# Kernel optimization log

Hardware: AMD Instinct MI355X
Metric: run time of the kernel (lower is better)

Reference implementation:

```python
import jax, jax.numpy as jnp
import numpy as np

B, N, D, E, K = 4, 4096, 768, 8, 2
H = 4 * D
LN_EPS = 1e-5


def setup_inputs() -> dict:
    key = jax.random.key(0)
    ks = jax.random.split(key, 9)
    s_d = 1.0 / np.sqrt(D)
    s_h = 1.0 / np.sqrt(H)
    return {
        "x": jax.random.normal(ks[0], (B, N, D), dtype=jnp.float32),
        "router_w": jax.random.normal(ks[1], (D, E), dtype=jnp.float32) * s_d,
        "router_b": jnp.zeros((E,), dtype=jnp.float32),
        "w1": jax.random.normal(ks[2], (E, D, H), dtype=jnp.float32) * s_d,
        "b1": jnp.zeros((E, H), dtype=jnp.float32),
        "w2": jax.random.normal(ks[3], (E, H, D), dtype=jnp.float32) * s_h,
        "b2": jnp.zeros((E, D), dtype=jnp.float32),
        "gamma": jnp.ones((D,), dtype=jnp.float32),
        "beta": jnp.zeros((D,), dtype=jnp.float32),
    }


def reference(x, router_w, router_b, w1, b1, w2, b2, gamma, beta):
    # Router logits and top-k gating (softmax over top-k values, in fp32)
    logits = jnp.einsum("bnd,de->bne", x, router_w) + router_b
    topv, topi = jax.lax.top_k(logits, K)                       # [B,N,K]
    w = jax.nn.softmax(topv.astype(jnp.float32), axis=-1).astype(x.dtype)
    # Per-token per-expert combine weight: [B,N,E]
    onehot = (topi[..., None] == jnp.arange(E)).astype(x.dtype)  # [B,N,K,E]
    we = jnp.einsum("bnk,bnke->bne", w, onehot)
    # Dense per-expert FFN, weighted combine (loop over small fixed E)
    out = jnp.zeros_like(x)
    for e in range(E):
        h = jax.nn.gelu(jnp.einsum("bnd,dh->bnh", x, w1[e]) + b1[e],
                        approximate=False)                      # exact GELU like torch
        y_e = jnp.einsum("bnh,hd->bnd", h, w2[e]) + b2[e]
        out = out + y_e * we[..., e:e + 1]
    # Residual + LayerNorm
    y = x + out
    mu = jnp.mean(y, axis=-1, keepdims=True)
    var = jnp.mean((y - mu) ** 2, axis=-1, keepdims=True)
    return (y - mu) * jax.lax.rsqrt(var + LN_EPS) * gamma + beta
```

## Files before the change

### kernel.cpp

```cpp
#include <hip/hip_runtime.h>
#include <hip/hip_bf16.h>
#include <math.h>

#define T_TOK 16384
#define DIM 768
#define NE 8
#define HID 3072
#define PADT 33792
#define CHUNK 8192
#define NCHUNK 5
#define NSLOT (T_TOK * 2)

typedef unsigned short u16;
typedef __attribute__((ext_vector_type(8))) short bf16x8;
typedef __attribute__((ext_vector_type(4))) float f32x4;

__device__ __forceinline__ u16 f2bf(float f) {
  union { float f; unsigned u; } v; v.f = f;
  unsigned r = v.u + 0x7FFF + ((v.u >> 16) & 1);
  return (u16)(r >> 16);
}

__device__ __forceinline__ float bf2f(u16 u) {
  union { unsigned u; float f; } v; v.u = ((unsigned)u) << 16; return v.f;
}

__device__ __forceinline__ void async16(void* lds, const void* g) {
  __builtin_amdgcn_global_load_lds((const __attribute__((address_space(1))) void*)g,
                                   (__attribute__((address_space(3))) void*)lds, 16, 0, 0);
}

__device__ __forceinline__ float gelu_f(float v) {
  float z = fabsf(v) * 0.70710678118f;
  float t = __builtin_amdgcn_rcpf(1.f + 0.3275911f * z);
  float p = t * (0.254829592f +
            t * (-0.284496736f +
            t * (1.421413741f +
            t * (-1.453152027f +
            t * 1.061405429f))));
  float e = __expf(-z * z);
  float erfz = fmaf(-p, e, 1.f);
  float s = copysignf(erfz, v);
  return 0.5f * v * (1.f + s);
}

__global__ __launch_bounds__(256) void cvt_x_kernel(const float* __restrict__ x,
                                                    u16* __restrict__ xb) {
  int i = blockIdx.x * 256 + threadIdx.x;
  if (i < T_TOK * DIM / 4) {
    float4 v = ((const float4*)x)[i];
    ushort4 o = make_ushort4(f2bf(v.x), f2bf(v.y), f2bf(v.z), f2bf(v.w));
    ((ushort4*)xb)[i] = o;
  }
}

__global__ __launch_bounds__(256) void transpose_cvt(const float* __restrict__ in,
                                                     u16* __restrict__ outp, int R, int C) {
  __shared__ float tile[32][33];
  int e = blockIdx.z;
  int c0 = blockIdx.x * 32, r0 = blockIdx.y * 32;
  int tx = threadIdx.x & 31, ty = threadIdx.x >> 5;
  const float* ip = in + (size_t)e * R * C;
  u16* op = outp + (size_t)e * R * C;
#pragma unroll
  for (int i = 0; i < 4; ++i)
    tile[ty + i * 8][tx] = ip[(size_t)(r0 + ty + i * 8) * C + c0 + tx];
  __syncthreads();
#pragma unroll
  for (int i = 0; i < 4; ++i)
    op[(size_t)(c0 + ty + i * 8) * R + r0 + tx] = f2bf(tile[tx][ty + i * 8]);
}

__global__ __launch_bounds__(256) void router_kernel(
    const float* __restrict__ x, const float* __restrict__ rw,
    const float* __restrict__ rb, int* __restrict__ idxb,
    float* __restrict__ wtb) {
  __shared__ float rwt[NE * DIM];
  for (int i = threadIdx.x; i < NE * DIM; i += 256) {
    int d = i >> 3, e = i & 7;
    rwt[e * DIM + d] = rw[i];
  }
  __syncthreads();
  int lane = threadIdx.x & 63, wv = threadIdx.x >> 6;
#pragma unroll 1
  for (int it = 0; it < 8; ++it) {
    int t = blockIdx.x * 32 + wv * 8 + it;
    const float4* xr = (const float4*)(x + (size_t)t * DIM);
    float acc[NE];
#pragma unroll
    for (int e = 0; e < NE; ++e) acc[e] = 0.f;
#pragma unroll
    for (int i = 0; i < 3; ++i) {
      float4 xv = xr[lane + i * 64];
#pragma unroll
      for (int e = 0; e < NE; ++e) {
        float4 w4 = ((const float4*)(rwt + e * DIM))[lane + i * 64];
        acc[e] += xv.x * w4.x + xv.y * w4.y + xv.z * w4.z + xv.w * w4.w;
      }
    }
#pragma unroll
    for (int e = 0; e < NE; ++e)
      for (int off = 32; off; off >>= 1) acc[e] += __shfl_down(acc[e], off);
    if (lane == 0) {
      float lg[NE];
#pragma unroll
      for (int e = 0; e < NE; ++e) lg[e] = acc[e] + rb[e];
      int i0 = 0;
#pragma unroll
      for (int e = 1; e < NE; ++e) if (lg[e] > lg[i0]) i0 = e;
      int i1 = -1;
#pragma unroll
      for (int e = 0; e < NE; ++e)
        if (e != i0 && (i1 < 0 || lg[e] > lg[i1])) i1 = e;
      float ee = expf(lg[i1] - lg[i0]);
      float w0 = 1.f / (1.f + ee);
      float w1 = ee / (1.f + ee);
      idxb[t * 2] = i0; idxb[t * 2 + 1] = i1;
      wtb[t * 2] = w0; wtb[t * 2 + 1] = w1;
    }
  }
}

__global__ __launch_bounds__(256) void hist_kernel(const int* __restrict__ idxb,
                                                   int* __restrict__ whist) {
  int wv = threadIdx.x >> 6, lane = threadIdx.x & 63;
  int g = blockIdx.x * 4 + wv;
  int cnt = 0;
#pragma unroll
  for (int j = 0; j < 2; ++j) {
    int e = idxb[g * 128 + j * 64 + lane];
#pragma unroll
    for (int ex = 0; ex < NE; ++ex) {
      unsigned long long m = __ballot(e == ex);
      if (lane == ex) cnt += __popcll(m);
    }
  }
  if (lane < NE) whist[g * NE + lane] = cnt;
}

__global__ __launch_bounds__(256) void scan_kernel(const int* __restrict__ whist,
                                                   int* __restrict__ gbase,
                                                   int* __restrict__ offsets,
                                                   int* __restrict__ counts) {
  __shared__ int sgb[256 * NE];
  __shared__ int tot[NE], soff[NE + 1];
  int tid = threadIdx.x;
  if (tid < NE) {
    int run = 0;
    for (int g = 0; g < 256; ++g) { sgb[g * NE + tid] = run; run += whist[g * NE + tid]; }
    tot[tid] = run; counts[tid] = run;
  }
  __syncthreads();
  if (tid == 0) {
    int off = 0;
    for (int e = 0; e < NE; ++e) {
      soff[e] = off; offsets[e] = off;
      off += (tot[e] + 127) & ~127;
    }
    soff[NE] = off; offsets[NE] = off;
  }
  __syncthreads();
  for (int i = tid; i < 256 * NE; i += 256) gbase[i] = sgb[i] + soff[i & 7];
}

__global__ __launch_bounds__(256) void scatter_kernel(
    const int* __restrict__ idxb, const int* __restrict__ gbase,
    int* __restrict__ g_tok, int* __restrict__ pairpos) {
  int wv = threadIdx.x >> 6, lane = threadIdx.x & 63;
  int g = blockIdx.x * 4 + wv;
  int run = (lane < NE) ? gbase[g * NE + lane] : 0;
  unsigned long long ltm = (1ull << lane) - 1ull;
#pragma unroll
  for (int j = 0; j < 2; ++j) {
    int slot = g * 128 + j * 64 + lane;
    int e = idxb[slot];
    int myrank = 0;
#pragma unroll
    for (int ex = 0; ex < NE; ++ex) {
      unsigned long long m = __ballot(e == ex);
      int b = __shfl(run, ex);
      if (e == ex) myrank = b + __popcll(m & ltm);
      if (lane == ex) run += __popcll(m);
    }
    g_tok[myrank] = slot >> 1;
    pairpos[slot] = myrank;
  }
}

__global__ __launch_bounds__(256, 2) void gemm1_kernel(
    const u16* __restrict__ xb, const u16* __restrict__ w1t,
    const float* __restrict__ b1, const int* __restrict__ g_tok,
    const int* __restrict__ offsets, const int* __restrict__ counts,
    u16* __restrict__ hbuf, int g0) {
  const int g = g0 + blockIdx.x * 128;
  int e = -1;
#pragma unroll
  for (int i = 0; i < NE; ++i)
    if (g >= offsets[i] && g < offsets[i + 1]) e = i;
  if (e < 0) return;
  const int off = offsets[e];
  const int cnt = counts[e];
  const int r0 = g - off;
  if (r0 >= cnt) return;
  const int n0 = blockIdx.y * 128;

  __shared__ u16 As[128 * 64];
  __shared__ u16 Bs[128 * 64];

  const int tid = threadIdx.x;
  const int lane = tid & 63;
  const int wv = tid >> 6;
  const int wr = wv >> 1, wc = wv & 1;
  const int scol = (((lane & 7) ^ (lane >> 3)) * 8);

  const u16* agp[4];
  const u16* bgp[4];
#pragma unroll
  for (int i = 0; i < 4; ++i) {
    int r = r0 + wv * 32 + i * 8 + (lane >> 3);
    int rr = r < cnt ? r : cnt - 1;
    int tok = g_tok[off + rr];
    agp[i] = xb + (size_t)tok * DIM + scol;
    int n = n0 + wv * 32 + i * 8 + (lane >> 3);
    bgp[i] = w1t + ((size_t)e * HID + n) * DIM + scol;
  }

  f32x4 acc[4][4];
#pragma unroll
  for (int i = 0; i < 4; ++i)
#pragma unroll
    for (int j = 0; j < 4; ++j) acc[i][j] = (f32x4){0.f, 0.f, 0.f, 0.f};

  for (int kt = 0; kt < DIM; kt += 64) {
#pragma unroll
    for (int i = 0; i < 4; ++i) {
      async16(&As[(wv * 32 + i * 8) * 64], agp[i] + kt);
      async16(&Bs[(wv * 32 + i * 8) * 64], bgp[i] + kt);
    }
    __syncthreads();
#pragma unroll
    for (int kk = 0; kk < 2; ++kk) {
      bf16x8 af[4], bfr[4];
#pragma unroll
      for (int i = 0; i < 4; ++i)
        af[i] = *(const bf16x8*)&As[(wr * 64 + i * 16 + (lane & 15)) * 64 +
                                    (((kk * 4 + (lane >> 4)) ^ (lane & 7)) * 8)];
#pragma unroll
      for (int j = 0; j < 4; ++j)
        bfr[j] = *(const bf16x8*)&Bs[(wc * 64 + j * 16 + (lane & 15)) * 64 +
                                     (((kk * 4 + (lane >> 4)) ^ (lane & 7)) * 8)];
#pragma unroll
      for (int i = 0; i < 4; ++i)
#pragma unroll
        for (int j = 0; j < 4; ++j)
          acc[i][j] = __builtin_amdgcn_mfma_f32_16x16x32_bf16(af[i], bfr[j], acc[i][j], 0, 0, 0);
    }
    __syncthreads();
  }

#pragma unroll
  for (int i = 0; i < 4; ++i) {
#pragma unroll
    for (int j = 0; j < 4; ++j) {
      int col = n0 + wc * 64 + j * 16 + (lane & 15);
      float bias = b1[e * HID + col];
#pragma unroll
      for (int rg = 0; rg < 4; ++rg) {
        int rloc = wr * 64 + i * 16 + (lane >> 4) * 4 + rg;
        if (r0 + rloc < cnt) {
          float v = gelu_f(acc[i][j][rg] + bias);
          hbuf[(size_t)(g - g0 + rloc) * HID + col] = f2bf(v);
        }
      }
    }
  }
}

__global__ __launch_bounds__(256, 2) void gemm2_kernel(
    const u16* __restrict__ hbuf, const u16* __restrict__ w2t,
    const float* __restrict__ b2, const int* __restrict__ offsets,
    const int* __restrict__ counts, u16* __restrict__ ygb, int g0) {
  const int g = g0 + blockIdx.x * 128;
  int e = -1;
#pragma unroll
  for (int i = 0; i < NE; ++i)
    if (g >= offsets[i] && g < offsets[i + 1]) e = i;
  if (e < 0) return;
  const int off = offsets[e];
  const int cnt = counts[e];
  const int r0 = g - off;
  if (r0 >= cnt) return;
  const int n0 = blockIdx.y * 128;

  __shared__ u16 As[128 * 64];
  __shared__ u16 Bs[128 * 64];

  const int tid = threadIdx.x;
  const int lane = tid & 63;
  const int wv = tid >> 6;
  const int wr = wv >> 1, wc = wv & 1;
  const int scol = (((lane & 7) ^ (lane >> 3)) * 8);

  const u16* agp[4];
  const u16* bgp[4];
#pragma unroll
  for (int i = 0; i < 4; ++i) {
    int r = r0 + wv * 32 + i * 8 + (lane >> 3);
    int rr = r < cnt ? r : cnt - 1;
    agp[i] = hbuf + (size_t)(off + rr - g0) * HID + scol;
    int n = n0 + wv * 32 + i * 8 + (lane >> 3);
    bgp[i] = w2t + ((size_t)e * DIM + n) * HID + scol;
  }

  f32x4 acc[4][4];
#pragma unroll
  for (int i = 0; i < 4; ++i)
#pragma unroll
    for (int j = 0; j < 4; ++j) acc[i][j] = (f32x4){0.f, 0.f, 0.f, 0.f};

  for (int kt = 0; kt < HID; kt += 64) {
#pragma unroll
    for (int i = 0; i < 4; ++i) {
      async16(&As[(wv * 32 + i * 8) * 64], agp[i] + kt);
      async16(&Bs[(wv * 32 + i * 8) * 64], bgp[i] + kt);
    }
    __syncthreads();
#pragma unroll
    for (int kk = 0; kk < 2; ++kk) {
      bf16x8 af[4], bfr[4];
#pragma unroll
      for (int i = 0; i < 4; ++i)
        af[i] = *(const bf16x8*)&As[(wr * 64 + i * 16 + (lane & 15)) * 64 +
                                    (((kk * 4 + (lane >> 4)) ^ (lane & 7)) * 8)];
#pragma unroll
      for (int j = 0; j < 4; ++j)
        bfr[j] = *(const bf16x8*)&Bs[(wc * 64 + j * 16 + (lane & 15)) * 64 +
                                     (((kk * 4 + (lane >> 4)) ^ (lane & 7)) * 8)];
#pragma unroll
      for (int i = 0; i < 4; ++i)
#pragma unroll
        for (int j = 0; j < 4; ++j)
          acc[i][j] = __builtin_amdgcn_mfma_f32_16x16x32_bf16(af[i], bfr[j], acc[i][j], 0, 0, 0);
    }
    __syncthreads();
  }

#pragma unroll
  for (int i = 0; i < 4; ++i) {
#pragma unroll
    for (int j = 0; j < 4; ++j) {
      int col = n0 + wc * 64 + j * 16 + (lane & 15);
      float bias = b2[e * DIM + col];
#pragma unroll
      for (int rg = 0; rg < 4; ++rg) {
        int rloc = wr * 64 + i * 16 + (lane >> 4) * 4 + rg;
        if (r0 + rloc < cnt)
          ygb[(size_t)(off + r0 + rloc) * DIM + col] = f2bf(acc[i][j][rg] + bias);
      }
    }
  }
}

__global__ __launch_bounds__(256) void combine_ln_kernel(
    const float* __restrict__ x, const u16* __restrict__ ygb,
    const int* __restrict__ pairpos, const float* __restrict__ wtb,
    const float* __restrict__ gamma, const float* __restrict__ beta,
    float* __restrict__ out) {
  int t = blockIdx.x;
  int p0 = pairpos[t * 2], p1 = pairpos[t * 2 + 1];
  float w0 = wtb[t * 2], w1 = wtb[t * 2 + 1];
  const float* xr = x + (size_t)t * DIM;
  const u16* y0 = ygb + (size_t)p0 * DIM;
  const u16* y1 = ygb + (size_t)p1 * DIM;
  float y[3];
  float s = 0.f, s2 = 0.f;
#pragma unroll
  for (int i = 0; i < 3; ++i) {
    int d = threadIdx.x + i * 256;
    float v = xr[d] + w0 * bf2f(y0[d]) + w1 * bf2f(y1[d]);
    y[i] = v; s += v; s2 += v * v;
  }
  for (int o = 32; o; o >>= 1) { s += __shfl_down(s, o); s2 += __shfl_down(s2, o); }
  __shared__ float red[8];
  int lane = threadIdx.x & 63, wv = threadIdx.x >> 6;
  if (lane == 0) { red[wv] = s; red[4 + wv] = s2; }
  __syncthreads();
  s = red[0] + red[1] + red[2] + red[3];
  s2 = red[4] + red[5] + red[6] + red[7];
  float mu = s * (1.f / DIM);
  float var = s2 * (1.f / DIM) - mu * mu;
  float inv = 1.f / sqrtf(var + 1e-5f);
#pragma unroll
  for (int i = 0; i < 3; ++i) {
    int d = threadIdx.x + i * 256;
    out[(size_t)t * DIM + d] = (y[i] - mu) * inv * gamma[d] + beta[d];
  }
}

extern "C" void kernel_launch(void* const* d_in, const int* in_sizes, int n_in,
                              void* d_out, int out_size, void* d_ws, size_t ws_size,
                              hipStream_t stream) {
  const float* x = (const float*)d_in[0];
  const float* rw = (const float*)d_in[1];
  const float* rb = (const float*)d_in[2];
  const float* w1 = (const float*)d_in[3];
  const float* b1 = (const float*)d_in[4];
  const float* w2 = (const float*)d_in[5];
  const float* b2 = (const float*)d_in[6];
  const float* gamma = (const float*)d_in[7];
  const float* beta = (const float*)d_in[8];
  float* out = (float*)d_out;

  char* p = (char*)d_ws;
  size_t o = 0;
  auto take = [&](size_t b) { void* q = (void*)(p + o); o += (b + 255) & ~((size_t)255); return q; };
  u16* xb = (u16*)take((size_t)T_TOK * DIM * 2);
  u16* w1t = (u16*)take((size_t)NE * HID * DIM * 2);
  u16* w2t = (u16*)take((size_t)NE * DIM * HID * 2);
  u16* hbuf = (u16*)take((size_t)CHUNK * HID * 2);
  u16* ygb = (u16*)take((size_t)PADT * DIM * 2);
  int* g_tok = (int*)take((size_t)PADT * 4);
  int* pairpos = (int*)take((size_t)NSLOT * 4);
  int* idxb = (int*)take((size_t)NSLOT * 4);
  float* wtb = (float*)take((size_t)NSLOT * 4);
  int* whist = (int*)take((size_t)256 * NE * 4);
  int* gbase = (int*)take((size_t)256 * NE * 4);
  int* counts = (int*)take(64);
  int* offsets = (int*)take(64);
  (void)in_sizes; (void)n_in; (void)out_size;

  if (o > ws_size) return;

  cvt_x_kernel<<<(T_TOK * DIM / 4 + 255) / 256, 256, 0, stream>>>(x, xb);
  transpose_cvt<<<dim3(HID / 32, DIM / 32, NE), 256, 0, stream>>>(w1, w1t, DIM, HID);
  transpose_cvt<<<dim3(DIM / 32, HID / 32, NE), 256, 0, stream>>>(w2, w2t, HID, DIM);
  router_kernel<<<512, 256, 0, stream>>>(x, rw, rb, idxb, wtb);
  hist_kernel<<<64, 256, 0, stream>>>(idxb, whist);
  scan_kernel<<<1, 256, 0, stream>>>(whist, gbase, offsets, counts);
  scatter_kernel<<<64, 256, 0, stream>>>(idxb, gbase, g_tok, pairpos);
  for (int c = 0; c < NCHUNK; ++c) {
    gemm1_kernel<<<dim3(CHUNK / 128, HID / 128), 256, 0, stream>>>(
        xb, w1t, b1, g_tok, offsets, counts, hbuf, c * CHUNK);
    gemm2_kernel<<<dim3(CHUNK / 128, DIM / 128), 256, 0, stream>>>(
        hbuf, w2t, b2, offsets, counts, ygb, c * CHUNK);
  }
  combine_ln_kernel<<<T_TOK, 256, 0, stream>>>(x, ygb, pairpos, wtb, gamma, beta, out);
}
```

Before: 684.5 us.

## Double-buffer GEMM LDS tiles, fuse x conversion into router, size chunks from workspace

Both expert GEMM kernels now double-buffer their LDS tiles. The next K-tile's async global-to-LDS loads are issued before computing the current one, with explicit vmcnt waits, raw barriers and raised wave priority around the MFMA block, so load latency overlaps compute. The bf16 conversion of x moves into the router kernel, which removes a separate launch and a second read of x. The hidden-buffer chunk is sized from the remaining workspace, which means fewer GEMM launch pairs. Doubled LDS use (64KB per block) may reduce occupancy below the two blocks per CU that the launch bounds target.

```diff
diff --git a/kernel.cpp b/kernel.cpp
--- a/kernel.cpp
+++ b/kernel.cpp
@@ -7,8 +7,6 @@
 #define NE 8
 #define HID 3072
 #define PADT 33792
-#define CHUNK 8192
-#define NCHUNK 5
 #define NSLOT (T_TOK * 2)
 
 typedef unsigned short u16;
@@ -44,16 +42,6 @@
   return 0.5f * v * (1.f + s);
 }
 
-__global__ __launch_bounds__(256) void cvt_x_kernel(const float* __restrict__ x,
-                                                    u16* __restrict__ xb) {
-  int i = blockIdx.x * 256 + threadIdx.x;
-  if (i < T_TOK * DIM / 4) {
-    float4 v = ((const float4*)x)[i];
-    ushort4 o = make_ushort4(f2bf(v.x), f2bf(v.y), f2bf(v.z), f2bf(v.w));
-    ((ushort4*)xb)[i] = o;
-  }
-}
-
 __global__ __launch_bounds__(256) void transpose_cvt(const float* __restrict__ in,
                                                      u16* __restrict__ outp, int R, int C) {
   __shared__ float tile[32][33];
@@ -74,7 +62,7 @@
 __global__ __launch_bounds__(256) void router_kernel(
     const float* __restrict__ x, const float* __restrict__ rw,
     const float* __restrict__ rb, int* __restrict__ idxb,
-    float* __restrict__ wtb) {
+    float* __restrict__ wtb, u16* __restrict__ xb) {
   __shared__ float rwt[NE * DIM];
   for (int i = threadIdx.x; i < NE * DIM; i += 256) {
     int d = i >> 3, e = i & 7;
@@ -86,16 +74,22 @@
   for (int it = 0; it < 8; ++it) {
     int t = blockIdx.x * 32 + wv * 8 + it;
     const float4* xr = (const float4*)(x + (size_t)t * DIM);
+    float4 xv[3];
+#pragma unroll
+    for (int i = 0; i < 3; ++i) xv[i] = xr[lane + i * 64];
+    ushort4* xo = (ushort4*)(xb + (size_t)t * DIM);
+#pragma unroll
+    for (int i = 0; i < 3; ++i)
+      xo[lane + i * 64] = make_ushort4(f2bf(xv[i].x), f2bf(xv[i].y), f2bf(xv[i].z), f2bf(xv[i].w));
     float acc[NE];
 #pragma unroll
     for (int e = 0; e < NE; ++e) acc[e] = 0.f;
 #pragma unroll
     for (int i = 0; i < 3; ++i) {
-      float4 xv = xr[lane + i * 64];
 #pragma unroll
       for (int e = 0; e < NE; ++e) {
         float4 w4 = ((const float4*)(rwt + e * DIM))[lane + i * 64];
-        acc[e] += xv.x * w4.x + xv.y * w4.y + xv.z * w4.z + xv.w * w4.w;
+        acc[e] += xv[i].x * w4.x + xv[i].y * w4.y + xv[i].z * w4.z + xv[i].w * w4.w;
       }
     }
 #pragma unroll
@@ -204,8 +198,8 @@
   if (r0 >= cnt) return;
   const int n0 = blockIdx.y * 128;
 
-  __shared__ u16 As[128 * 64];
-  __shared__ u16 Bs[128 * 64];
+  __shared__ u16 As[2][128 * 64];
+  __shared__ u16 Bs[2][128 * 64];
 
   const int tid = threadIdx.x;
   const int lane = tid & 63;
@@ -231,31 +225,49 @@
 #pragma unroll
     for (int j = 0; j < 4; ++j) acc[i][j] = (f32x4){0.f, 0.f, 0.f, 0.f};
 
-  for (int kt = 0; kt < DIM; kt += 64) {
-#pragma unroll
-    for (int i = 0; i < 4; ++i) {
-      async16(&As[(wv * 32 + i * 8) * 64], agp[i] + kt);
-      async16(&Bs[(wv * 32 + i * 8) * 64], bgp[i] + kt);
-    }
-    __syncthreads();
+  const int NT = DIM / 64;
+#pragma unroll
+  for (int i = 0; i < 4; ++i) {
+    async16(&As[0][(wv * 32 + i * 8) * 64], agp[i]);
+    async16(&Bs[0][(wv * 32 + i * 8) * 64], bgp[i]);
+  }
+#pragma unroll 1
+  for (int t = 0; t < NT; ++t) {
+    const int cur = t & 1;
+    if (t + 1 < NT) {
+      const int nxt = cur ^ 1;
+      const int kt = (t + 1) * 64;
+#pragma unroll
+      for (int i = 0; i < 4; ++i) {
+        async16(&As[nxt][(wv * 32 + i * 8) * 64], agp[i] + kt);
+        async16(&Bs[nxt][(wv * 32 + i * 8) * 64], bgp[i] + kt);
+      }
+      asm volatile("s_waitcnt vmcnt(8)" ::: "memory");
+    } else {
+      asm volatile("s_waitcnt vmcnt(0)" ::: "memory");
+    }
+    __builtin_amdgcn_s_barrier();
+    __builtin_amdgcn_s_setprio(1);
 #pragma unroll
     for (int kk = 0; kk < 2; ++kk) {
       bf16x8 af[4], bfr[4];
 #pragma unroll
       for (int i = 0; i < 4; ++i)
-        af[i] = *(const bf16x8*)&As[(wr * 64 + i * 16 + (lane & 15)) * 64 +
-                                    (((kk * 4 + (lane >> 4)) ^ (lane & 7)) * 8)];
+        af[i] = *(const bf16x8*)&As[cur][(wr * 64 + i * 16 + (lane & 15)) * 64 +
+                                        (((kk * 4 + (lane >> 4)) ^ (lane & 7)) * 8)];
 #pragma unroll
       for (int j = 0; j < 4; ++j)
-        bfr[j] = *(const bf16x8*)&Bs[(wc * 64 + j * 16 + (lane & 15)) * 64 +
-                                     (((kk * 4 + (lane >> 4)) ^ (lane & 7)) * 8)];
+        bfr[j] = *(const bf16x8*)&Bs[cur][(wc * 64 + j * 16 + (lane & 15)) * 64 +
+                                         (((kk * 4 + (lane >> 4)) ^ (lane & 7)) * 8)];
 #pragma unroll
       for (int i = 0; i < 4; ++i)
 #pragma unroll
         for (int j = 0; j < 4; ++j)
           acc[i][j] = __builtin_amdgcn_mfma_f32_16x16x32_bf16(af[i], bfr[j], acc[i][j], 0, 0, 0);
     }
-    __syncthreads();
+    __builtin_amdgcn_s_setprio(0);
+    asm volatile("" ::: "memory");
+    __builtin_amdgcn_s_barrier();
   }
 
 #pragma unroll
@@ -292,8 +304,8 @@
   if (r0 >= cnt) return;
   const int n0 = blockIdx.y * 128;
 
-  __shared__ u16 As[128 * 64];
-  __shared__ u16 Bs[128 * 64];
+  __shared__ u16 As[2][128 * 64];
+  __shared__ u16 Bs[2][128 * 64];
 
   const int tid = threadIdx.x;
   const int lane = tid & 63;
@@ -318,31 +330,49 @@
 #pragma unroll
     for (int j = 0; j < 4; ++j) acc[i][j] = (f32x4){0.f, 0.f, 0.f, 0.f};
 
-  for (int kt = 0; kt < HID; kt += 64) {
-#pragma unroll
-    for (int i = 0; i < 4; ++i) {
-      async16(&As[(wv * 32 + i * 8) * 64], agp[i] + kt);
-      async16(&Bs[(wv * 32 + i * 8) * 64], bgp[i] + kt);
-    }
-    __syncthreads();
+  const int NT = HID / 64;
+#pragma unroll
+  for (int i = 0; i < 4; ++i) {
+    async16(&As[0][(wv * 32 + i * 8) * 64], agp[i]);
+    async16(&Bs[0][(wv * 32 + i * 8) * 64], bgp[i]);
+  }
+#pragma unroll 1
+  for (int t = 0; t < NT; ++t) {
+    const int cur = t & 1;
+    if (t + 1 < NT) {
+      const int nxt = cur ^ 1;
+      const int kt = (t + 1) * 64;
+#pragma unroll
+      for (int i = 0; i < 4; ++i) {
+        async16(&As[nxt][(wv * 32 + i * 8) * 64], agp[i] + kt);
+        async16(&Bs[nxt][(wv * 32 + i * 8) * 64], bgp[i] + kt);
+      }
+      asm volatile("s_waitcnt vmcnt(8)" ::: "memory");
+    } else {
+      asm volatile("s_waitcnt vmcnt(0)" ::: "memory");
+    }
+    __builtin_amdgcn_s_barrier();
+    __builtin_amdgcn_s_setprio(1);
 #pragma unroll
     for (int kk = 0; kk < 2; ++kk) {
       bf16x8 af[4], bfr[4];
 #pragma unroll
       for (int i = 0; i < 4; ++i)
-        af[i] = *(const bf16x8*)&As[(wr * 64 + i * 16 + (lane & 15)) * 64 +
-                                    (((kk * 4 + (lane >> 4)) ^ (lane & 7)) * 8)];
+        af[i] = *(const bf16x8*)&As[cur][(wr * 64 + i * 16 + (lane & 15)) * 64 +
+                                        (((kk * 4 + (lane >> 4)) ^ (lane & 7)) * 8)];
 #pragma unroll
       for (int j = 0; j < 4; ++j)
-        bfr[j] = *(const bf16x8*)&Bs[(wc * 64 + j * 16 + (lane & 15)) * 64 +
-                                     (((kk * 4 + (lane >> 4)) ^ (lane & 7)) * 8)];
+        bfr[j] = *(const bf16x8*)&Bs[cur][(wc * 64 + j * 16 + (lane & 15)) * 64 +
+                                         (((kk * 4 + (lane >> 4)) ^ (lane & 7)) * 8)];
 #pragma unroll
       for (int i = 0; i < 4; ++i)
 #pragma unroll
         for (int j = 0; j < 4; ++j)
           acc[i][j] = __builtin_amdgcn_mfma_f32_16x16x32_bf16(af[i], bfr[j], acc[i][j], 0, 0, 0);
     }
-    __syncthreads();
+    __builtin_amdgcn_s_setprio(0);
+    asm volatile("" ::: "memory");
+    __builtin_amdgcn_s_barrier();
   }
 
 #pragma unroll
@@ -417,7 +447,6 @@
   u16* xb = (u16*)take((size_t)T_TOK * DIM * 2);
   u16* w1t = (u16*)take((size_t)NE * HID * DIM * 2);
   u16* w2t = (u16*)take((size_t)NE * DIM * HID * 2);
-  u16* hbuf = (u16*)take((size_t)CHUNK * HID * 2);
   u16* ygb = (u16*)take((size_t)PADT * DIM * 2);
   int* g_tok = (int*)take((size_t)PADT * 4);
   int* pairpos = (int*)take((size_t)NSLOT * 4);
@@ -429,20 +458,25 @@
   int* offsets = (int*)take(64);
   (void)in_sizes; (void)n_in; (void)out_size;
 
-  if (o > ws_size) return;
-
-  cvt_x_kernel<<<(T_TOK * DIM / 4 + 255) / 256, 256, 0, stream>>>(x, xb);
+  if (o + 256 > ws_size) return;
+  size_t rem = ws_size - o;
+  u16* hbuf = (u16*)take(rem);
+  int chunk = (int)(rem / ((size_t)HID * 2));
+  if (chunk > PADT) chunk = PADT;
+  chunk &= ~127;
+  if (chunk < 128) return;
+
+  router_kernel<<<512, 256, 0, stream>>>(x, rw, rb, idxb, wtb, xb);
   transpose_cvt<<<dim3(HID / 32, DIM / 32, NE), 256, 0, stream>>>(w1, w1t, DIM, HID);
   transpose_cvt<<<dim3(DIM / 32, HID / 32, NE), 256, 0, stream>>>(w2, w2t, HID, DIM);
-  router_kernel<<<512, 256, 0, stream>>>(x, rw, rb, idxb, wtb);
   hist_kernel<<<64, 256, 0, stream>>>(idxb, whist);
   scan_kernel<<<1, 256, 0, stream>>>(whist, gbase, offsets, counts);
   scatter_kernel<<<64, 256, 0, stream>>>(idxb, gbase, g_tok, pairpos);
-  for (int c = 0; c < NCHUNK; ++c) {
-    gemm1_kernel<<<dim3(CHUNK / 128, HID / 128), 256, 0, stream>>>(
-        xb, w1t, b1, g_tok, offsets, counts, hbuf, c * CHUNK);
-    gemm2_kernel<<<dim3(CHUNK / 128, DIM / 128), 256, 0, stream>>>(
-        hbuf, w2t, b2, offsets, counts, ygb, c * CHUNK);
+  for (int g0 = 0; g0 < PADT; g0 += chunk) {
+    gemm1_kernel<<<dim3(chunk / 128, HID / 128), 256, 0, stream>>>(
+        xb, w1t, b1, g_tok, offsets, counts, hbuf, g0);
+    gemm2_kernel<<<dim3(chunk / 128, DIM / 128), 256, 0, stream>>>(
+        hbuf, w2t, b2, offsets, counts, ygb, g0);
   }
   combine_ln_kernel<<<T_TOK, 256, 0, stream>>>(x, ygb, pairpos, wtb, gamma, beta, out);
 }
```

Result: slower. 766.1 us (+11.9%).
